# Kernel tuning notes

Measured on AMD Instinct MI355X. Metric: run time of the kernel, lower is better.

Reference implementation:

```python
import jax, jax.numpy as jnp
import numpy as np


def setup_inputs() -> dict:
    key = jax.random.key(0)
    k1, k2, k3, k4 = jax.random.split(key, 4)
    T, B, I, H = 512, 64, 1024, 1024
    sigma = 0.01
    return {
        "inputs": jax.random.normal(k1, (T, B, I), dtype=jnp.float32),
        "W_xh": jax.random.normal(k2, (I, H), dtype=jnp.float32) * sigma,
        "W_hh": jax.random.normal(k3, (H, H), dtype=jnp.float32) * sigma,
        "b_h": jnp.zeros((H,), dtype=jnp.float32),
    }


def reference(inputs, W_xh, W_hh, b_h):
    # Tanh RNN: h_t = tanh(x_t @ W_xh + h_{t-1} @ W_hh + b_h), h_{-1} = 0.
    # (state=None in the torch module contributes 0 on the first step,
    #  identical to an all-zeros initial state.)
    B, H = inputs.shape[1], W_hh.shape[0]
    # Precompute the input projections for all timesteps in one big GEMM.
    xW = jnp.einsum("tbi,ih->tbh", inputs, W_xh) + b_h  # [T, B, H]

    def step(h, xw_t):
        h = jnp.tanh(xw_t + h @ W_hh)
        return h, h

    h0 = jnp.zeros((B, H), dtype=inputs.dtype)
    last_state, outputs = jax.lax.scan(step, h0, xW)
    return outputs, last_state
```

## Files before the change

### kernel.cpp

```cpp
#include <hip/hip_runtime.h>
#include <hip/hip_bf16.h>
#include <stdint.h>

typedef __attribute__((ext_vector_type(8))) short short8;
typedef __attribute__((ext_vector_type(4))) short short4v;
typedef __attribute__((ext_vector_type(4))) float f32x4;
typedef __attribute__((ext_vector_type(4))) int int4v;

#define T_STEPS 512
#define BATCH 64
#define HDIM 1024
#define MROWS (T_STEPS * BATCH)

__device__ __forceinline__ unsigned short f2bf(float f) {
  unsigned int u = __float_as_uint(f);
  u += 0x7FFFu + ((u >> 16) & 1u);
  return (unsigned short)(u >> 16);
}

__global__ __launch_bounds__(256) void transpose_cvt(const float* __restrict__ src,
                                                     unsigned short* __restrict__ dst) {
  __shared__ unsigned short tile[32][36];
  int b = blockIdx.x;
  int tr = b >> 5, tc = b & 31;
  int t = threadIdx.x;
  int i = t >> 3, j4 = (t & 7) << 2;
  const float4 v = *(const float4*)(src + (size_t)(tr * 32 + i) * 1024 + tc * 32 + j4);
  tile[i][j4 + 0] = f2bf(v.x);
  tile[i][j4 + 1] = f2bf(v.y);
  tile[i][j4 + 2] = f2bf(v.z);
  tile[i][j4 + 3] = f2bf(v.w);
  __syncthreads();
  int c = t >> 3, r4 = (t & 7) << 2;
  short4v o;
  o[0] = (short)tile[r4 + 0][c];
  o[1] = (short)tile[r4 + 1][c];
  o[2] = (short)tile[r4 + 2][c];
  o[3] = (short)tile[r4 + 3][c];
  *(short4v*)(dst + (size_t)(tc * 32 + c) * 1024 + tr * 32 + r4) = o;
}

__global__ __launch_bounds__(256, 2) void xw_gemm(const float* __restrict__ A,
                                                  const unsigned short* __restrict__ BT,
                                                  const float* __restrict__ bias,
                                                  float* __restrict__ C) {
  __shared__ unsigned short As[128][40];
  __shared__ unsigned short Bs[128][40];
  int b = blockIdx.x;
  int swz = (b & 7) * 256 + (b >> 3);
  int tn = swz & 7, tm = swz >> 3;
  int t = threadIdx.x, lane = t & 63, wave = t >> 6;
  int l15 = lane & 15, l4 = lane >> 4;
  int wm = wave >> 1, wn = wave & 1;

  f32x4 acc[4][4];
#pragma unroll
  for (int i = 0; i < 4; ++i)
#pragma unroll
    for (int j = 0; j < 4; ++j) acc[i][j] = (f32x4){0.f, 0.f, 0.f, 0.f};

  int sm = t >> 1, sh = (t & 1) << 4;
  const float* a_src = A + (size_t)(tm * 128 + sm) * 1024 + sh;
  const unsigned short* b_src = BT + (size_t)(tn * 128 + sm) * 1024 + sh;

  for (int kt = 0; kt < 32; ++kt) {
    float4 av0 = *(const float4*)(a_src + kt * 32 + 0);
    float4 av1 = *(const float4*)(a_src + kt * 32 + 4);
    float4 av2 = *(const float4*)(a_src + kt * 32 + 8);
    float4 av3 = *(const float4*)(a_src + kt * 32 + 12);
    short8 w0, w1;
    w0[0] = (short)f2bf(av0.x); w0[1] = (short)f2bf(av0.y);
    w0[2] = (short)f2bf(av0.z); w0[3] = (short)f2bf(av0.w);
    w0[4] = (short)f2bf(av1.x); w0[5] = (short)f2bf(av1.y);
    w0[6] = (short)f2bf(av1.z); w0[7] = (short)f2bf(av1.w);
    w1[0] = (short)f2bf(av2.x); w1[1] = (short)f2bf(av2.y);
    w1[2] = (short)f2bf(av2.z); w1[3] = (short)f2bf(av2.w);
    w1[4] = (short)f2bf(av3.x); w1[5] = (short)f2bf(av3.y);
    w1[6] = (short)f2bf(av3.z); w1[7] = (short)f2bf(av3.w);
    *(short8*)&As[sm][sh] = w0;
    *(short8*)&As[sm][sh + 8] = w1;
    short8 bv0 = *(const short8*)(b_src + kt * 32 + 0);
    short8 bv1 = *(const short8*)(b_src + kt * 32 + 8);
    *(short8*)&Bs[sm][sh] = bv0;
    *(short8*)&Bs[sm][sh + 8] = bv1;
    __syncthreads();

    short8 af[4], bfr[4];
#pragma unroll
    for (int i = 0; i < 4; ++i) af[i] = *(const short8*)&As[wm * 64 + i * 16 + l15][8 * l4];
#pragma unroll
    for (int j = 0; j < 4; ++j) bfr[j] = *(const short8*)&Bs[wn * 64 + j * 16 + l15][8 * l4];
#pragma unroll
    for (int i = 0; i < 4; ++i)
#pragma unroll
      for (int j = 0; j < 4; ++j)
        acc[i][j] = __builtin_amdgcn_mfma_f32_16x16x32_bf16(af[i], bfr[j], acc[i][j], 0, 0, 0);
    __syncthreads();
  }

#pragma unroll
  for (int i = 0; i < 4; ++i) {
    int row0 = tm * 128 + wm * 64 + i * 16 + l4 * 4;
#pragma unroll
    for (int j = 0; j < 4; ++j) {
      int col = tn * 128 + wn * 64 + j * 16 + l15;
      float bv = bias[col];
#pragma unroll
      for (int r = 0; r < 4; ++r)
        C[(size_t)(row0 + r) * 1024 + col] = acc[i][j][r] + bv;
    }
  }
}

__device__ __forceinline__ void coh_store_dword(int* p, int v) {
  asm volatile("global_store_dword %0, %1, off sc0 sc1" ::"v"(p), "v"(v) : "memory");
}
__device__ __forceinline__ void coh_load_dwordx4_issue(int4v* dst, const int* p) {
  asm volatile("global_load_dwordx4 %0, %1, off sc0 sc1" : "=&v"(*dst) : "v"(p) : "memory");
}

__global__ __launch_bounds__(256, 1) void rnn_scan(const unsigned short* __restrict__ whhT,
                                                   float* __restrict__ out,
                                                   int* __restrict__ hbuf) {
  int wg = blockIdx.x;
  int bg = wg >> 4;
  int cg = wg & 15;
  int t = threadIdx.x, lane = t & 63, wave = t >> 6;
  int l15 = lane & 15, l4 = lane >> 4;

  __shared__ __align__(16) float red[2][4][64][4][4];

  short8 wfrag[4][8];
#pragma unroll
  for (int c = 0; c < 4; ++c)
#pragma unroll
    for (int m = 0; m < 8; ++m)
      wfrag[c][m] = *(const short8*)(whhT + (size_t)(64 * cg + 16 * c + l15) * 1024 +
                                     256 * wave + 32 * m + 8 * l4);

  int colw = 64 * cg + 16 * wave + l15;

  for (int s = 0; s < T_STEPS; ++s) {
    float xw[4];
#pragma unroll
    for (int r = 0; r < 4; ++r)
      xw[r] = out[((size_t)s * BATCH + bg * 16 + l4 * 4 + r) * HDIM + colw];

    f32x4 acc[4];
#pragma unroll
    for (int c = 0; c < 4; ++c) acc[c] = (f32x4){0.f, 0.f, 0.f, 0.f};

    if (s > 0) {
      const unsigned tagv = (unsigned)s;
      const int* base = hbuf + (((s - 1) & 1) << 16) + (16 * bg + l15) * 1024 + 256 * wave;
      const int* sp = base + 64 * l4 + 4 * l15;
      int4v q[16];
      for (;;) {
        for (;;) {
          int4v sv;
          coh_load_dwordx4_issue(&sv, sp);
          asm volatile("s_waitcnt vmcnt(0)" ::: "memory");
          unsigned bad = (((unsigned)sv[0] >> 16) ^ tagv) | (((unsigned)sv[1] >> 16) ^ tagv) |
                         (((unsigned)sv[2] >> 16) ^ tagv) | (((unsigned)sv[3] >> 16) ^ tagv);
          if (__all(bad == 0)) break;
          __builtin_amdgcn_s_sleep(2);
        }
#pragma unroll
        for (int jj = 0; jj < 4; ++jj) {
          const int* fb = base + 64 * jj + 8 * l4;
          coh_load_dwordx4_issue(&q[jj * 4 + 0], fb);
          coh_load_dwordx4_issue(&q[jj * 4 + 1], fb + 4);
          coh_load_dwordx4_issue(&q[jj * 4 + 2], fb + 32);
          coh_load_dwordx4_issue(&q[jj * 4 + 3], fb + 36);
        }
        asm volatile("s_waitcnt vmcnt(0)" ::: "memory");
        __builtin_amdgcn_sched_barrier(0);
        unsigned bad = 0;
#pragma unroll
        for (int i = 0; i < 16; ++i) {
          bad |= (((unsigned)q[i][0] >> 16) ^ tagv) | (((unsigned)q[i][1] >> 16) ^ tagv) |
                 (((unsigned)q[i][2] >> 16) ^ tagv) | (((unsigned)q[i][3] >> 16) ^ tagv);
        }
        if (__all(bad == 0)) break;
        __builtin_amdgcn_s_sleep(1);
      }
#pragma unroll
      for (int jj = 0; jj < 4; ++jj) {
        int4v a0 = q[jj * 4 + 0], a1 = q[jj * 4 + 1], a2 = q[jj * 4 + 2], a3 = q[jj * 4 + 3];
        int4v p0, p1;
        p0[0] = (a0[0] & 0xffff) | (a0[1] << 16);
        p0[1] = (a0[2] & 0xffff) | (a0[3] << 16);
        p0[2] = (a1[0] & 0xffff) | (a1[1] << 16);
        p0[3] = (a1[2] & 0xffff) | (a1[3] << 16);
        p1[0] = (a2[0] & 0xffff) | (a2[1] << 16);
        p1[1] = (a2[2] & 0xffff) | (a2[3] << 16);
        p1[2] = (a3[0] & 0xffff) | (a3[1] << 16);
        p1[3] = (a3[2] & 0xffff) | (a3[3] << 16);
#pragma unroll
        for (int c = 0; c < 4; ++c) {
          acc[c] = __builtin_amdgcn_mfma_f32_16x16x32_bf16(*(short8*)&p0, wfrag[c][2 * jj],
                                                           acc[c], 0, 0, 0);
          acc[c] = __builtin_amdgcn_mfma_f32_16x16x32_bf16(*(short8*)&p1, wfrag[c][2 * jj + 1],
                                                           acc[c], 0, 0, 0);
        }
      }
    }

    int p = s & 1;
#pragma unroll
    for (int c = 0; c < 4; ++c) *(f32x4*)&red[p][wave][lane][c][0] = acc[c];
    __syncthreads();
    f32x4 hsum;
#pragma unroll
    for (int r = 0; r < 4; ++r)
      hsum[r] = red[p][0][lane][wave][r] + red[p][1][lane][wave][r] +
                red[p][2][lane][wave][r] + red[p][3][lane][wave][r];

#pragma unroll
    for (int r = 0; r < 4; ++r) {
      int row = bg * 16 + l4 * 4 + r;
      size_t oidx = ((size_t)s * BATCH + row) * HDIM + colw;
      float hv = tanhf(xw[r] + hsum[r]);
      out[oidx] = hv;
      if (s != T_STEPS - 1)
        coh_store_dword(hbuf + ((s & 1) << 16) + row * 1024 + colw,
                        (int)(((unsigned)(s + 1) << 16) | (unsigned)f2bf(hv)));
      else
        out[(size_t)MROWS * HDIM + (size_t)row * HDIM + colw] = hv;
    }
  }
}

extern "C" void kernel_launch(void* const* d_in, const int* in_sizes, int n_in,
                              void* d_out, int out_size, void* d_ws, size_t ws_size,
                              hipStream_t stream) {
  const float* inp = (const float*)d_in[0];
  const float* wxh = (const float*)d_in[1];
  const float* whh = (const float*)d_in[2];
  const float* bh  = (const float*)d_in[3];
  float* out = (float*)d_out;

  char* ws = (char*)d_ws;
  unsigned short* whhT = (unsigned short*)(ws);
  unsigned short* wxhT = (unsigned short*)(ws + (2u << 20));
  int* hbuf = (int*)(ws + (4u << 20));

  hipMemsetAsync(hbuf, 0, 2u * BATCH * HDIM * sizeof(int), stream);
  transpose_cvt<<<1024, 256, 0, stream>>>(whh, whhT);
  transpose_cvt<<<1024, 256, 0, stream>>>(wxh, wxhT);
  xw_gemm<<<2048, 256, 0, stream>>>(inp, wxhT, bh, out);
  rnn_scan<<<64, 256, 0, stream>>>(whhT, out, hbuf);
}
```

Measured before the change: 2.667 ms.

## Fuse input projection GEMM into the recurrent scan kernel

Removes the separate xW GEMM kernel and computes each step's x_t @ W_xh inside the 64-block recurrent kernel, with W_xh fragments held in registers next to W_hh. This avoids writing and re-reading the full xW tensor and removes a kernel launch. The input-projection MFMAs run before the spin-wait, so they can overlap the cross-block wait. The spin-wait is also restructured into per-chunk polling with an iteration cap, which could let a block read stale data. The trade-off is that the projection work now runs on only 64 blocks, each holding twice the register-resident weights, which may limit occupancy.

After: 3.671 ms. 37.7% more time.

```diff
diff --git a/kernel.cpp b/kernel.cpp
--- a/kernel.cpp
+++ b/kernel.cpp
@@ -40,88 +40,19 @@
   *(short4v*)(dst + (size_t)(tc * 32 + c) * 1024 + tr * 32 + r4) = o;
 }
 
-__global__ __launch_bounds__(256, 2) void xw_gemm(const float* __restrict__ A,
-                                                  const unsigned short* __restrict__ BT,
-                                                  const float* __restrict__ bias,
-                                                  float* __restrict__ C) {
-  __shared__ unsigned short As[128][40];
-  __shared__ unsigned short Bs[128][40];
-  int b = blockIdx.x;
-  int swz = (b & 7) * 256 + (b >> 3);
-  int tn = swz & 7, tm = swz >> 3;
-  int t = threadIdx.x, lane = t & 63, wave = t >> 6;
-  int l15 = lane & 15, l4 = lane >> 4;
-  int wm = wave >> 1, wn = wave & 1;
-
-  f32x4 acc[4][4];
-#pragma unroll
-  for (int i = 0; i < 4; ++i)
-#pragma unroll
-    for (int j = 0; j < 4; ++j) acc[i][j] = (f32x4){0.f, 0.f, 0.f, 0.f};
-
-  int sm = t >> 1, sh = (t & 1) << 4;
-  const float* a_src = A + (size_t)(tm * 128 + sm) * 1024 + sh;
-  const unsigned short* b_src = BT + (size_t)(tn * 128 + sm) * 1024 + sh;
-
-  for (int kt = 0; kt < 32; ++kt) {
-    float4 av0 = *(const float4*)(a_src + kt * 32 + 0);
-    float4 av1 = *(const float4*)(a_src + kt * 32 + 4);
-    float4 av2 = *(const float4*)(a_src + kt * 32 + 8);
-    float4 av3 = *(const float4*)(a_src + kt * 32 + 12);
-    short8 w0, w1;
-    w0[0] = (short)f2bf(av0.x); w0[1] = (short)f2bf(av0.y);
-    w0[2] = (short)f2bf(av0.z); w0[3] = (short)f2bf(av0.w);
-    w0[4] = (short)f2bf(av1.x); w0[5] = (short)f2bf(av1.y);
-    w0[6] = (short)f2bf(av1.z); w0[7] = (short)f2bf(av1.w);
-    w1[0] = (short)f2bf(av2.x); w1[1] = (short)f2bf(av2.y);
-    w1[2] = (short)f2bf(av2.z); w1[3] = (short)f2bf(av2.w);
-    w1[4] = (short)f2bf(av3.x); w1[5] = (short)f2bf(av3.y);
-    w1[6] = (short)f2bf(av3.z); w1[7] = (short)f2bf(av3.w);
-    *(short8*)&As[sm][sh] = w0;
-    *(short8*)&As[sm][sh + 8] = w1;
-    short8 bv0 = *(const short8*)(b_src + kt * 32 + 0);
-    short8 bv1 = *(const short8*)(b_src + kt * 32 + 8);
-    *(short8*)&Bs[sm][sh] = bv0;
-    *(short8*)&Bs[sm][sh + 8] = bv1;
-    __syncthreads();
-
-    short8 af[4], bfr[4];
-#pragma unroll
-    for (int i = 0; i < 4; ++i) af[i] = *(const short8*)&As[wm * 64 + i * 16 + l15][8 * l4];
-#pragma unroll
-    for (int j = 0; j < 4; ++j) bfr[j] = *(const short8*)&Bs[wn * 64 + j * 16 + l15][8 * l4];
-#pragma unroll
-    for (int i = 0; i < 4; ++i)
-#pragma unroll
-      for (int j = 0; j < 4; ++j)
-        acc[i][j] = __builtin_amdgcn_mfma_f32_16x16x32_bf16(af[i], bfr[j], acc[i][j], 0, 0, 0);
-    __syncthreads();
-  }
-
-#pragma unroll
-  for (int i = 0; i < 4; ++i) {
-    int row0 = tm * 128 + wm * 64 + i * 16 + l4 * 4;
-#pragma unroll
-    for (int j = 0; j < 4; ++j) {
-      int col = tn * 128 + wn * 64 + j * 16 + l15;
-      float bv = bias[col];
-#pragma unroll
-      for (int r = 0; r < 4; ++r)
-        C[(size_t)(row0 + r) * 1024 + col] = acc[i][j][r] + bv;
-    }
-  }
-}
-
 __device__ __forceinline__ void coh_store_dword(int* p, int v) {
   asm volatile("global_store_dword %0, %1, off sc0 sc1" ::"v"(p), "v"(v) : "memory");
 }
-__device__ __forceinline__ void coh_load_dwordx4_issue(int4v* dst, const int* p) {
+__device__ __forceinline__ void coh_load_x4(int4v* dst, const int* p) {
   asm volatile("global_load_dwordx4 %0, %1, off sc0 sc1" : "=&v"(*dst) : "v"(p) : "memory");
 }
 
-__global__ __launch_bounds__(256, 1) void rnn_scan(const unsigned short* __restrict__ whhT,
-                                                   float* __restrict__ out,
-                                                   int* __restrict__ hbuf) {
+__global__ __launch_bounds__(256, 1) void rnn_fused(const unsigned short* __restrict__ whhT,
+                                                    const unsigned short* __restrict__ wxhT,
+                                                    const float* __restrict__ inp,
+                                                    const float* __restrict__ bh,
+                                                    float* __restrict__ out,
+                                                    int* __restrict__ hb2) {
   int wg = blockIdx.x;
   int bg = wg >> 4;
   int cg = wg & 15;
@@ -131,71 +62,73 @@
   __shared__ __align__(16) float red[2][4][64][4][4];
 
   short8 wfrag[4][8];
+  short8 xfrag[4][8];
 #pragma unroll
   for (int c = 0; c < 4; ++c)
 #pragma unroll
-    for (int m = 0; m < 8; ++m)
-      wfrag[c][m] = *(const short8*)(whhT + (size_t)(64 * cg + 16 * c + l15) * 1024 +
-                                     256 * wave + 32 * m + 8 * l4);
+    for (int m = 0; m < 8; ++m) {
+      size_t off = (size_t)(64 * cg + 16 * c + l15) * 1024 + 256 * wave + 32 * m + 8 * l4;
+      wfrag[c][m] = *(const short8*)(whhT + off);
+      xfrag[c][m] = *(const short8*)(wxhT + off);
+    }
 
   int colw = 64 * cg + 16 * wave + l15;
+  float bias = bh[colw];
 
   for (int s = 0; s < T_STEPS; ++s) {
-    float xw[4];
-#pragma unroll
-    for (int r = 0; r < 4; ++r)
-      xw[r] = out[((size_t)s * BATCH + bg * 16 + l4 * 4 + r) * HDIM + colw];
-
     f32x4 acc[4];
 #pragma unroll
     for (int c = 0; c < 4; ++c) acc[c] = (f32x4){0.f, 0.f, 0.f, 0.f};
 
+    {
+      const float* ibase = inp + ((size_t)s * BATCH + 16 * bg + l15) * HDIM + 256 * wave + 8 * l4;
+#pragma unroll
+      for (int m = 0; m < 8; ++m) {
+        float4 u0 = *(const float4*)(ibase + 32 * m);
+        float4 u1 = *(const float4*)(ibase + 32 * m + 4);
+        short8 af;
+        af[0] = (short)f2bf(u0.x); af[1] = (short)f2bf(u0.y);
+        af[2] = (short)f2bf(u0.z); af[3] = (short)f2bf(u0.w);
+        af[4] = (short)f2bf(u1.x); af[5] = (short)f2bf(u1.y);
+        af[6] = (short)f2bf(u1.z); af[7] = (short)f2bf(u1.w);
+#pragma unroll
+        for (int c = 0; c < 4; ++c)
+          acc[c] = __builtin_amdgcn_mfma_f32_16x16x32_bf16(af, xfrag[c][m], acc[c], 0, 0, 0);
+      }
+    }
+
     if (s > 0) {
       const unsigned tagv = (unsigned)s;
-      const int* base = hbuf + (((s - 1) & 1) << 16) + (16 * bg + l15) * 1024 + 256 * wave;
-      const int* sp = base + 64 * l4 + 4 * l15;
-      int4v q[16];
-      for (;;) {
-        for (;;) {
-          int4v sv;
-          coh_load_dwordx4_issue(&sv, sp);
-          asm volatile("s_waitcnt vmcnt(0)" ::: "memory");
-          unsigned bad = (((unsigned)sv[0] >> 16) ^ tagv) | (((unsigned)sv[1] >> 16) ^ tagv) |
-                         (((unsigned)sv[2] >> 16) ^ tagv) | (((unsigned)sv[3] >> 16) ^ tagv);
-          if (__all(bad == 0)) break;
-          __builtin_amdgcn_s_sleep(2);
-        }
-#pragma unroll
-        for (int jj = 0; jj < 4; ++jj) {
-          const int* fb = base + 64 * jj + 8 * l4;
-          coh_load_dwordx4_issue(&q[jj * 4 + 0], fb);
-          coh_load_dwordx4_issue(&q[jj * 4 + 1], fb + 4);
-          coh_load_dwordx4_issue(&q[jj * 4 + 2], fb + 32);
-          coh_load_dwordx4_issue(&q[jj * 4 + 3], fb + 36);
-        }
-        asm volatile("s_waitcnt vmcnt(0)" ::: "memory");
-        __builtin_amdgcn_sched_barrier(0);
-        unsigned bad = 0;
-#pragma unroll
-        for (int i = 0; i < 16; ++i) {
-          bad |= (((unsigned)q[i][0] >> 16) ^ tagv) | (((unsigned)q[i][1] >> 16) ^ tagv) |
-                 (((unsigned)q[i][2] >> 16) ^ tagv) | (((unsigned)q[i][3] >> 16) ^ tagv);
-        }
-        if (__all(bad == 0)) break;
-        __builtin_amdgcn_s_sleep(1);
-      }
+      const int* base = hb2 + (((s - 1) & 1) << 16) + (16 * bg + l15) * 1024 + 256 * wave;
 #pragma unroll
       for (int jj = 0; jj < 4; ++jj) {
-        int4v a0 = q[jj * 4 + 0], a1 = q[jj * 4 + 1], a2 = q[jj * 4 + 2], a3 = q[jj * 4 + 3];
+        const int* fb = base + 64 * jj + 8 * l4;
+        int4v c0, c1, c2, c3;
+        int guard = 0;
+        for (;;) {
+          coh_load_x4(&c0, fb);
+          coh_load_x4(&c1, fb + 4);
+          coh_load_x4(&c2, fb + 32);
+          coh_load_x4(&c3, fb + 36);
+          asm volatile("s_waitcnt vmcnt(0)" ::: "memory");
+          __builtin_amdgcn_sched_barrier(0);
+          unsigned bad = 0;
+#pragma unroll
+          for (int e = 0; e < 4; ++e)
+            bad |= (((unsigned)c0[e] >> 16) ^ tagv) | (((unsigned)c1[e] >> 16) ^ tagv) |
+                   (((unsigned)c2[e] >> 16) ^ tagv) | (((unsigned)c3[e] >> 16) ^ tagv);
+          if (__all(bad == 0)) break;
+          if (++guard > 16384) break;
+        }
         int4v p0, p1;
-        p0[0] = (a0[0] & 0xffff) | (a0[1] << 16);
-        p0[1] = (a0[2] & 0xffff) | (a0[3] << 16);
-        p0[2] = (a1[0] & 0xffff) | (a1[1] << 16);
-        p0[3] = (a1[2] & 0xffff) | (a1[3] << 16);
-        p1[0] = (a2[0] & 0xffff) | (a2[1] << 16);
-        p1[1] = (a2[2] & 0xffff) | (a2[3] << 16);
-        p1[2] = (a3[0] & 0xffff) | (a3[1] << 16);
-        p1[3] = (a3[2] & 0xffff) | (a3[3] << 16);
+        p0[0] = (c0[0] & 0xffff) | (c0[1] << 16);
+        p0[1] = (c0[2] & 0xffff) | (c0[3] << 16);
+        p0[2] = (c1[0] & 0xffff) | (c1[1] << 16);
+        p0[3] = (c1[2] & 0xffff) | (c1[3] << 16);
+        p1[0] = (c2[0] & 0xffff) | (c2[1] << 16);
+        p1[1] = (c2[2] & 0xffff) | (c2[3] << 16);
+        p1[2] = (c3[0] & 0xffff) | (c3[1] << 16);
+        p1[3] = (c3[2] & 0xffff) | (c3[3] << 16);
 #pragma unroll
         for (int c = 0; c < 4; ++c) {
           acc[c] = __builtin_amdgcn_mfma_f32_16x16x32_bf16(*(short8*)&p0, wfrag[c][2 * jj],
@@ -220,10 +153,10 @@
     for (int r = 0; r < 4; ++r) {
       int row = bg * 16 + l4 * 4 + r;
       size_t oidx = ((size_t)s * BATCH + row) * HDIM + colw;
-      float hv = tanhf(xw[r] + hsum[r]);
+      float hv = tanhf(hsum[r] + bias);
       out[oidx] = hv;
       if (s != T_STEPS - 1)
-        coh_store_dword(hbuf + ((s & 1) << 16) + row * 1024 + colw,
+        coh_store_dword(hb2 + ((s & 1) << 16) + row * 1024 + colw,
                         (int)(((unsigned)(s + 1) << 16) | (unsigned)f2bf(hv)));
       else
         out[(size_t)MROWS * HDIM + (size_t)row * HDIM + colw] = hv;
@@ -243,11 +176,10 @@
   char* ws = (char*)d_ws;
   unsigned short* whhT = (unsigned short*)(ws);
   unsigned short* wxhT = (unsigned short*)(ws + (2u << 20));
-  int* hbuf = (int*)(ws + (4u << 20));
+  int* hb2 = (int*)(ws + (4u << 20));
 
-  hipMemsetAsync(hbuf, 0, 2u * BATCH * HDIM * sizeof(int), stream);
+  hipMemsetAsync(hb2, 0, 2u * BATCH * HDIM * sizeof(int), stream);
   transpose_cvt<<<1024, 256, 0, stream>>>(whh, whhT);
   transpose_cvt<<<1024, 256, 0, stream>>>(wxh, wxhT);
-  xw_gemm<<<2048, 256, 0, stream>>>(inp, wxhT, bh, out);
-  rnn_scan<<<64, 256, 0, stream>>>(whhT, out, hbuf);
+  rnn_fused<<<64, 256, 0, stream>>>(whhT, wxhT, inp, bh, out, hb2);
 }
```
